# Performance work log

Measured on AMD Instinct MI355X. Metric: run time of the kernel, lower is better.

Reference implementation:

```python
import jax, jax.numpy as jnp
import numpy as np

N_ENTITIES = 500000
N_RELATIONS = 200
EMBED_DIM = 128
RELATION_DIM = 128  # must equal EMBED_DIM for the reshape in calculate_score
BATCH = 16384
KG_L2_LAMBDA = 1e-5


def _xavier_uniform(key, shape):
    fan_in, fan_out = shape[0], shape[1]
    limit = float(np.sqrt(6.0 / (fan_in + fan_out)))
    return jax.random.uniform(key, shape, jnp.float32, -limit, limit)


def setup_inputs() -> dict:
    key = jax.random.key(0)
    k1, k2, k3, k4, k5, k6 = jax.random.split(key, 6)
    entity_embed = _xavier_uniform(k1, (N_ENTITIES, EMBED_DIM))
    relation_embed = _xavier_uniform(k2, (N_RELATIONS, RELATION_DIM * EMBED_DIM))
    h = jax.random.randint(k3, (BATCH,), 0, N_ENTITIES, dtype=jnp.int64)
    r = jax.random.randint(k4, (BATCH,), 0, N_RELATIONS, dtype=jnp.int64)
    pos_t = jax.random.randint(k5, (BATCH,), 0, N_ENTITIES, dtype=jnp.int64)
    neg_t = jax.random.randint(k6, (BATCH,), 0, N_ENTITIES, dtype=jnp.int64)
    return {"h": h, "r": r, "pos_t": pos_t, "neg_t": neg_t,
            "entity_embed": entity_embed, "relation_embed": relation_embed}


def _l2_loss_mean(x):
    # mean over batch of sum(x^2, dim=1) / 2
    return jnp.mean(jnp.sum(x * x, axis=1) / 2.0)


def _score(h_e, t_e, r_mat):
    # r_mat: (B, relation_dim, embed_dim); tr = r @ t : (B, embed_dim)
    tr = jnp.einsum('bde,be->bd', r_mat, t_e)
    return -jnp.sum(h_e * tr, axis=-1)  # (B,)


def reference(h, r, pos_t, neg_t, entity_embed, relation_embed):
    r_embed = relation_embed[r]                     # (B, R*D)
    head_embed = entity_embed[h]                    # (B, D)
    tail_pos_embed = entity_embed[pos_t]            # (B, D)
    tail_neg_embed = entity_embed[neg_t]            # (B, D)
    r_mat = r_embed.reshape(-1, RELATION_DIM, EMBED_DIM)
    pos_score = _score(head_embed, tail_pos_embed, r_mat)
    neg_score = _score(head_embed, tail_neg_embed, r_mat)
    triplet_loss = jnp.mean(-jax.nn.log_sigmoid(neg_score - pos_score))
    l2_loss = (_l2_loss_mean(head_embed) + _l2_loss_mean(r_embed)
               + _l2_loss_mean(tail_pos_embed) + _l2_loss_mean(tail_neg_embed))
    return triplet_loss + KG_L2_LAMBDA * l2_loss
```

## Files before the change

### kernel.cpp

```cpp
#include <hip/hip_runtime.h>
#include <math.h>

#define BATCH 16384
#define EDIM 128
#define RD (EDIM * EDIM)
#define NREL 200
#define SPLIT 4
#define NBLK (NREL * SPLIT)
#define NTHR 256
#define QUARTER (BATCH / SPLIT)
#define PERT (QUARTER / NTHR)
#define EB 8
#define LISTCAP 256


__device__ __forceinline__ int load_idx(const void* p, int b, int is64) {
    if (is64) return (int)((const long long*)p)[b];
    return ((const int*)p)[b];
}

__global__ __launch_bounds__(NTHR) void rescal_kernel(
    const void* __restrict__ hI, const void* __restrict__ rI,
    const void* __restrict__ pI, const void* __restrict__ nI,
    const float* __restrict__ ent, const float* __restrict__ rel,
    float* __restrict__ csum) {
    const int t = threadIdx.x;
    const int bid = blockIdx.x;
    const int rid = bid >> 2;
    const int qtr = bid & 3;
    const int lane = t & 63;
    const int wave = t >> 6;
    const int c2 = lane * 2;

    __shared__ unsigned short list[LISTCAP];
    __shared__ unsigned int wtot[4], um4[4];
    __shared__ float wsum[4];

    unsigned int o = ((const unsigned int*)hI)[2 * t + 1] |
                     ((const unsigned int*)rI)[2 * t + 1] |
                     ((const unsigned int*)pI)[2 * t + 1] |
                     ((const unsigned int*)nI)[2 * t + 1];
#pragma unroll
    for (int off = 32; off; off >>= 1) o |= __shfl_xor(o, off, 64);
    if (lane == 0) um4[wave] = o;
    __syncthreads();
    const int is64 = ((um4[0] | um4[1] | um4[2] | um4[3]) == 0u) ? 1 : 0;

    const int base0 = qtr * QUARTER + t * PERT;
    int rv[PERT];
    int cl = 0;
#pragma unroll
    for (int j = 0; j < PERT; ++j) {
        rv[j] = load_idx(rI, base0 + j, is64);
        cl += (rv[j] == rid);
    }
    int incl = cl;
#pragma unroll
    for (int off = 1; off < 64; off <<= 1) {
        const int nv = __shfl_up(incl, off, 64);
        if (lane >= off) incl += nv;
    }
    if (lane == 63) wtot[wave] = (unsigned int)incl;
    __syncthreads();
    int base = 0, cnt = 0;
#pragma unroll
    for (int w = 0; w < 4; ++w) {
        const int wv = (int)wtot[w];
        base += (w < wave) ? wv : 0;
        cnt += wv;
    }
    if (cnt > LISTCAP) cnt = LISTCAP;
    {
        int rk = base + incl - cl;
#pragma unroll
        for (int j = 0; j < PERT; ++j) {
            if (rv[j] == rid) {
                if (rk < LISTCAP) list[rk] = (unsigned short)(base0 + j);
                ++rk;
            }
        }
    }
    __syncthreads();

    const int per_wave = (cnt + 3) >> 2;
    int lo = wave * per_wave;
    int hi = (wave + 1) * per_wave;
    if (lo > cnt) lo = cnt;
    if (hi > cnt) hi = cnt;

    const float* Rg = rel + (size_t)rid * RD;
    float lsum = 0.f;
    float r2w = 0.f;

    for (int e0 = lo; e0 < hi; e0 += EB) {
        int bidx[EB];
        const float* hrow[EB];
#pragma unroll
        for (int i = 0; i < EB; ++i) {
            int e = e0 + i;
            if (e >= hi) e = hi - 1;
            int b = (int)list[e];
            b = __builtin_amdgcn_readfirstlane(b);
            bidx[i] = b;
            int hix = load_idx(hI, b, is64);
            hix = __builtin_amdgcn_readfirstlane(hix);
            hrow[i] = ent + (size_t)hix * EDIM;
        }

        float2 acc[EB];
#pragma unroll
        for (int i = 0; i < EB; ++i) acc[i] = make_float2(0.f, 0.f);
        float r2p = 0.f;
#pragma unroll 4
        for (int db = 0; db < 32; ++db) {
            float4 hv0 = *(const float4*)(hrow[0] + db * 4);
            float4 hv1 = *(const float4*)(hrow[1] + db * 4);
            float4 hv2 = *(const float4*)(hrow[2] + db * 4);
            float4 hv3 = *(const float4*)(hrow[3] + db * 4);
            float4 hv4 = *(const float4*)(hrow[4] + db * 4);
            float4 hv5 = *(const float4*)(hrow[5] + db * 4);
            float4 hv6 = *(const float4*)(hrow[6] + db * 4);
            float4 hv7 = *(const float4*)(hrow[7] + db * 4);
#pragma unroll
            for (int jj = 0; jj < 4; ++jj) {
                const int d = db * 4 + jj;
                const float2 r2v = *(const float2*)(Rg + d * EDIM + c2);
                r2p = fmaf(r2v.x, r2v.x, fmaf(r2v.y, r2v.y, r2p));
                const float h0 = (jj == 0) ? hv0.x : (jj == 1) ? hv0.y : (jj == 2) ? hv0.z : hv0.w;
                const float h1 = (jj == 0) ? hv1.x : (jj == 1) ? hv1.y : (jj == 2) ? hv1.z : hv1.w;
                const float h2 = (jj == 0) ? hv2.x : (jj == 1) ? hv2.y : (jj == 2) ? hv2.z : hv2.w;
                const float h3 = (jj == 0) ? hv3.x : (jj == 1) ? hv3.y : (jj == 2) ? hv3.z : hv3.w;
                const float h4 = (jj == 0) ? hv4.x : (jj == 1) ? hv4.y : (jj == 2) ? hv4.z : hv4.w;
                const float h5 = (jj == 0) ? hv5.x : (jj == 1) ? hv5.y : (jj == 2) ? hv5.z : hv5.w;
                const float h6 = (jj == 0) ? hv6.x : (jj == 1) ? hv6.y : (jj == 2) ? hv6.z : hv6.w;
                const float h7 = (jj == 0) ? hv7.x : (jj == 1) ? hv7.y : (jj == 2) ? hv7.z : hv7.w;
                acc[0].x = fmaf(r2v.x, h0, acc[0].x); acc[0].y = fmaf(r2v.y, h0, acc[0].y);
                acc[1].x = fmaf(r2v.x, h1, acc[1].x); acc[1].y = fmaf(r2v.y, h1, acc[1].y);
                acc[2].x = fmaf(r2v.x, h2, acc[2].x); acc[2].y = fmaf(r2v.y, h2, acc[2].y);
                acc[3].x = fmaf(r2v.x, h3, acc[3].x); acc[3].y = fmaf(r2v.y, h3, acc[3].y);
                acc[4].x = fmaf(r2v.x, h4, acc[4].x); acc[4].y = fmaf(r2v.y, h4, acc[4].y);
                acc[5].x = fmaf(r2v.x, h5, acc[5].x); acc[5].y = fmaf(r2v.y, h5, acc[5].y);
                acc[6].x = fmaf(r2v.x, h6, acc[6].x); acc[6].y = fmaf(r2v.y, h6, acc[6].y);
                acc[7].x = fmaf(r2v.x, h7, acc[7].x); acc[7].y = fmaf(r2v.y, h7, acc[7].y);
            }
        }
#pragma unroll
        for (int off = 32; off; off >>= 1) r2p += __shfl_xor(r2p, off, 64);
        r2w = r2p;

#pragma unroll
        for (int i = 0; i < EB; ++i) {
            const int b = bidx[i];
            int pi = __builtin_amdgcn_readfirstlane(load_idx(pI, b, is64));
            int ni = __builtin_amdgcn_readfirstlane(load_idx(nI, b, is64));
            const float2 hv2 = *(const float2*)(hrow[i] + c2);
            const float2 tp2 = *(const float2*)(ent + (size_t)pi * EDIM + c2);
            const float2 tn2 = *(const float2*)(ent + (size_t)ni * EDIM + c2);
            float dp = acc[i].x * tp2.x + acc[i].y * tp2.y;
            float dn = acc[i].x * tn2.x + acc[i].y * tn2.y;
            float e2 = hv2.x * hv2.x + hv2.y * hv2.y + tp2.x * tp2.x + tp2.y * tp2.y +
                       tn2.x * tn2.x + tn2.y * tn2.y;
#pragma unroll
            for (int off = 32; off; off >>= 1) {
                dp += __shfl_xor(dp, off, 64);
                dn += __shfl_xor(dn, off, 64);
                e2 += __shfl_xor(e2, off, 64);
            }
            if (lane == 0 && (e0 + i) < hi) {
                const float x = dn - dp;
                const float spl = (x > 0.f) ? (x + log1pf(expf(-x))) : log1pf(expf(x));
                lsum += spl + 1e-5f * 0.5f * (e2 + r2w);
            }
        }
    }

    if (lane == 0) wsum[wave] = lsum;
    __syncthreads();
    if (t == 0) csum[bid] = wsum[0] + wsum[1] + wsum[2] + wsum[3];
}

__global__ __launch_bounds__(NTHR) void reduce_kernel(const float* __restrict__ csum,
                                                      float* __restrict__ out) {
    const int t = threadIdx.x;
    float a = 0.f;
    for (int i = t; i < NBLK; i += NTHR) a += csum[i];
#pragma unroll
    for (int off = 32; off; off >>= 1) a += __shfl_down(a, off, 64);
    __shared__ float sm[4];
    if ((t & 63) == 0) sm[t >> 6] = a;
    __syncthreads();
    if (t == 0) out[0] = (sm[0] + sm[1] + sm[2] + sm[3]) * (1.0f / (float)BATCH);
}

extern "C" void kernel_launch(void* const* d_in, const int* in_sizes, int n_in,
                              void* d_out, int out_size, void* d_ws, size_t ws_size,
                              hipStream_t stream) {
    const void* h = d_in[0];
    const void* r = d_in[1];
    const void* pt = d_in[2];
    const void* nt = d_in[3];
    const float* ent = (const float*)d_in[4];
    const float* rel = (const float*)d_in[5];
    float* csum = (float*)d_ws;

    rescal_kernel<<<NBLK, NTHR, 0, stream>>>(h, r, pt, nt, ent, rel, csum);
    reduce_kernel<<<1, NTHR, 0, stream>>>(csum, (float*)d_out);
}
```

Before: 56.57 us.

## Remap blocks to XCDs per relation and use ballot-based coalesced list compaction

Block IDs are remapped so all four quarter-blocks of a relation land on the same XCD (blockIdx mod 8), letting them share the 64KB relation matrix in that XCD's L2. The relation index scan now reads indices coalesced (stride NTHR) and builds the compacted list with wave ballots and popcounts instead of per-thread strided loads and a shuffle scan. The list now stores offsets relative to the quarter base. List order changes, which alters the floating-point summation order slightly.

```diff
diff --git a/kernel.cpp b/kernel.cpp
--- a/kernel.cpp
+++ b/kernel.cpp
@@ -9,7 +9,7 @@
 #define NBLK (NREL * SPLIT)
 #define NTHR 256
 #define QUARTER (BATCH / SPLIT)
-#define PERT (QUARTER / NTHR)
+#define NJ (QUARTER / NTHR)
 #define EB 8
 #define LISTCAP 256
 
@@ -25,15 +25,18 @@
     const float* __restrict__ ent, const float* __restrict__ rel,
     float* __restrict__ csum) {
     const int t = threadIdx.x;
-    const int bid = blockIdx.x;
-    const int rid = bid >> 2;
-    const int qtr = bid & 3;
+    const int bid0 = blockIdx.x;
+    const int xcd = bid0 & 7;
+    const int slot = bid0 >> 3;
+    const int rid = xcd + 8 * (slot >> 2);
+    const int qtr = slot & 3;
     const int lane = t & 63;
     const int wave = t >> 6;
     const int c2 = lane * 2;
 
     __shared__ unsigned short list[LISTCAP];
-    __shared__ unsigned int wtot[4], um4[4];
+    __shared__ unsigned int wtj[NJ][4];
+    __shared__ unsigned int um4[4];
     __shared__ float wsum[4];
 
     unsigned int o = ((const unsigned int*)hI)[2 * t + 1] |
@@ -46,39 +49,38 @@
     __syncthreads();
     const int is64 = ((um4[0] | um4[1] | um4[2] | um4[3]) == 0u) ? 1 : 0;
 
-    const int base0 = qtr * QUARTER + t * PERT;
-    int rv[PERT];
-    int cl = 0;
-#pragma unroll
-    for (int j = 0; j < PERT; ++j) {
-        rv[j] = load_idx(rI, base0 + j, is64);
-        cl += (rv[j] == rid);
+    const int qbase = qtr * QUARTER;
+    unsigned long long bal[NJ];
+#pragma unroll
+    for (int j = 0; j < NJ; ++j) {
+        const int rr = load_idx(rI, qbase + j * NTHR + t, is64);
+        bal[j] = __ballot(rr == rid);
+        if (lane == 0) wtj[j][wave] = (unsigned int)__popcll(bal[j]);
     }
-    int incl = cl;
-#pragma unroll
-    for (int off = 1; off < 64; off <<= 1) {
-        const int nv = __shfl_up(incl, off, 64);
-        if (lane >= off) incl += nv;
-    }
-    if (lane == 63) wtot[wave] = (unsigned int)incl;
-    __syncthreads();
-    int base = 0, cnt = 0;
-#pragma unroll
-    for (int w = 0; w < 4; ++w) {
-        const int wv = (int)wtot[w];
-        base += (w < wave) ? wv : 0;
-        cnt += wv;
-    }
-    if (cnt > LISTCAP) cnt = LISTCAP;
+    __syncthreads();
+    int cnt;
     {
-        int rk = base + incl - cl;
-#pragma unroll
-        for (int j = 0; j < PERT; ++j) {
-            if (rv[j] == rid) {
-                if (rk < LISTCAP) list[rk] = (unsigned short)(base0 + j);
-                ++rk;
-            }
-        }
+        unsigned int run = 0;
+        const unsigned long long ltmask = (lane == 63) ? ~0ull >> 1
+                                                       : (1ull << lane) - 1ull;
+#pragma unroll
+        for (int j = 0; j < NJ; ++j) {
+            unsigned int wpre = 0, tj = 0;
+#pragma unroll
+            for (int w = 0; w < 4; ++w) {
+                const unsigned int v = wtj[j][w];
+                tj += v;
+                wpre += (w < wave) ? v : 0;
+            }
+            if ((bal[j] >> lane) & 1ull) {
+                const unsigned int rank =
+                    run + wpre + (unsigned int)__popcll(bal[j] & ltmask);
+                if (rank < LISTCAP) list[rank] = (unsigned short)(j * NTHR + t);
+            }
+            run += tj;
+        }
+        cnt = (int)run;
+        if (cnt > LISTCAP) cnt = LISTCAP;
     }
     __syncthreads();
 
@@ -99,7 +101,7 @@
         for (int i = 0; i < EB; ++i) {
             int e = e0 + i;
             if (e >= hi) e = hi - 1;
-            int b = (int)list[e];
+            int b = qbase + (int)list[e];
             b = __builtin_amdgcn_readfirstlane(b);
             bidx[i] = b;
             int hix = load_idx(hI, b, is64);
@@ -176,7 +178,7 @@
 
     if (lane == 0) wsum[wave] = lsum;
     __syncthreads();
-    if (t == 0) csum[bid] = wsum[0] + wsum[1] + wsum[2] + wsum[3];
+    if (t == 0) csum[bid0] = wsum[0] + wsum[1] + wsum[2] + wsum[3];
 }
 
 __global__ __launch_bounds__(NTHR) void reduce_kernel(const float* __restrict__ csum,
```

After: 54.09 us. 4.4% less time.
